# Kernel tuning notes

Measured on AMD Instinct MI355X. Metric: run time of the kernel, lower is better.

## Reference

```python
import jax, jax.numpy as jnp
import numpy as np

EPS = 1e-5

def _bn2d(x, g, b, m, v):
    s = (1, -1, 1, 1)
    return (x - m.reshape(s)) * (g.reshape(s) * jax.lax.rsqrt(v.reshape(s) + EPS)) + b.reshape(s)

def _bn1d(x, g, b, m, v):
    return (x - m) * (g * jax.lax.rsqrt(v + EPS)) + b

def _conv3x3(x, w, b):
    y = jax.lax.conv_general_dilated(x, w, (1, 1), ((1, 1), (1, 1)),
                                     dimension_numbers=('NCHW', 'OIHW', 'NCHW'))
    return y + b.reshape(1, -1, 1, 1)

def setup_inputs() -> dict:
    key = jax.random.key(0)
    ks = iter(jax.random.split(key, 64))
    B = 512
    d = {}
    d['anchor'] = jax.random.normal(next(ks), (B, 1, 16, 8), jnp.float32)
    d['positive'] = jax.random.normal(next(ks), (B, 1, 16, 8), jnp.float32)
    d['negative'] = jax.random.normal(next(ks), (B, 1, 16, 8), jnp.float32)

    def bn_params(c):
        g = jax.random.normal(next(ks), (c,), jnp.float32) * 0.1 + 1.0
        b = jax.random.normal(next(ks), (c,), jnp.float32) * 0.1
        m = jax.random.normal(next(ks), (c,), jnp.float32) * 0.1
        v = jax.random.uniform(next(ks), (c,), jnp.float32, 0.5, 1.5)
        return g, b, m, v

    d['bn0_g'], d['bn0_b'], d['bn0_m'], d['bn0_v'] = bn_params(1)
    d['conv1_w'] = jax.random.normal(next(ks), (64, 1, 3, 3), jnp.float32) * 0.1
    d['conv1_b'] = jax.random.normal(next(ks), (64,), jnp.float32) * 0.1
    d['bn1_g'], d['bn1_b'], d['bn1_m'], d['bn1_v'] = bn_params(64)
    d['conv2_w'] = jax.random.normal(next(ks), (64, 64, 3, 3), jnp.float32) * 0.04
    d['conv2_b'] = jax.random.normal(next(ks), (64,), jnp.float32) * 0.1
    d['bn2_g'], d['bn2_b'], d['bn2_m'], d['bn2_v'] = bn_params(64)
    # locally-connected: kernel_size=1 -> per-position unshared channel mix (o,c,h,w)
    d['lc1_w'] = jax.random.normal(next(ks), (64, 64, 16, 8), jnp.float32) * 0.125
    d['bn3_g'], d['bn3_b'], d['bn3_m'], d['bn3_v'] = bn_params(64)
    d['lc2_w'] = jax.random.normal(next(ks), (64, 64, 16, 8), jnp.float32) * 0.125
    d['bn4_g'], d['bn4_b'], d['bn4_m'], d['bn4_v'] = bn_params(64)
    d['fc1_w'] = jax.random.normal(next(ks), (512, 8192), jnp.float32) * 0.01
    d['fc1_b'] = jax.random.normal(next(ks), (512,), jnp.float32) * 0.1
    d['bnf1_g'], d['bnf1_b'], d['bnf1_m'], d['bnf1_v'] = bn_params(512)
    d['fc2_w'] = jax.random.normal(next(ks), (512, 512), jnp.float32) * 0.04
    d['fc2_b'] = jax.random.normal(next(ks), (512,), jnp.float32) * 0.1
    d['bnf2_g'], d['bnf2_b'], d['bnf2_m'], d['bnf2_v'] = bn_params(512)
    d['fc3_w'] = jax.random.normal(next(ks), (128, 512), jnp.float32) * 0.04
    d['fc3_b'] = jax.random.normal(next(ks), (128,), jnp.float32) * 0.1
    d['bnf3_g'], d['bnf3_b'], d['bnf3_m'], d['bnf3_v'] = bn_params(128)
    d['out_w'] = jax.random.normal(next(ks), (128, 128), jnp.float32) * 0.09
    d['out_b'] = jax.random.normal(next(ks), (128,), jnp.float32) * 0.1
    return d

def _embedding(x, p):
    x = _bn2d(x, p['bn0_g'], p['bn0_b'], p['bn0_m'], p['bn0_v'])
    x = _conv3x3(x, p['conv1_w'], p['conv1_b'])
    x = jax.nn.relu(_bn2d(x, p['bn1_g'], p['bn1_b'], p['bn1_m'], p['bn1_v']))
    x = _conv3x3(x, p['conv2_w'], p['conv2_b'])
    x = jax.nn.relu(_bn2d(x, p['bn2_g'], p['bn2_b'], p['bn2_m'], p['bn2_v']))
    # locally connected (kernel 1): per-position channel mix, no huge unfold intermediate
    x = jnp.einsum('bchw,ochw->bohw', x, p['lc1_w'])
    x = jax.nn.relu(_bn2d(x, p['bn3_g'], p['bn3_b'], p['bn3_m'], p['bn3_v']))
    x = jnp.einsum('bchw,ochw->bohw', x, p['lc2_w'])
    x = jax.nn.relu(_bn2d(x, p['bn4_g'], p['bn4_b'], p['bn4_m'], p['bn4_v']))
    # dropout is identity in eval mode
    x = x.reshape(x.shape[0], -1)  # (B, 8192)
    x = x @ p['fc1_w'].T + p['fc1_b']
    x = jax.nn.relu(_bn1d(x, p['bnf1_g'], p['bnf1_b'], p['bnf1_m'], p['bnf1_v']))
    x = x @ p['fc2_w'].T + p['fc2_b']
    x = jax.nn.relu(_bn1d(x, p['bnf2_g'], p['bnf2_b'], p['bnf2_m'], p['bnf2_v']))
    x = x @ p['fc3_w'].T + p['fc3_b']
    x = jax.nn.relu(_bn1d(x, p['bnf3_g'], p['bnf3_b'], p['bnf3_m'], p['bnf3_v']))
    return x @ p['out_w'].T + p['out_b']

def reference(anchor, positive, negative,
              bn0_g, bn0_b, bn0_m, bn0_v,
              conv1_w, conv1_b, bn1_g, bn1_b, bn1_m, bn1_v,
              conv2_w, conv2_b, bn2_g, bn2_b, bn2_m, bn2_v,
              lc1_w, bn3_g, bn3_b, bn3_m, bn3_v,
              lc2_w, bn4_g, bn4_b, bn4_m, bn4_v,
              fc1_w, fc1_b, bnf1_g, bnf1_b, bnf1_m, bnf1_v,
              fc2_w, fc2_b, bnf2_g, bnf2_b, bnf2_m, bnf2_v,
              fc3_w, fc3_b, bnf3_g, bnf3_b, bnf3_m, bnf3_v,
              out_w, out_b):
    p = dict(bn0_g=bn0_g, bn0_b=bn0_b, bn0_m=bn0_m, bn0_v=bn0_v,
             conv1_w=conv1_w, conv1_b=conv1_b, bn1_g=bn1_g, bn1_b=bn1_b, bn1_m=bn1_m, bn1_v=bn1_v,
             conv2_w=conv2_w, conv2_b=conv2_b, bn2_g=bn2_g, bn2_b=bn2_b, bn2_m=bn2_m, bn2_v=bn2_v,
             lc1_w=lc1_w, bn3_g=bn3_g, bn3_b=bn3_b, bn3_m=bn3_m, bn3_v=bn3_v,
             lc2_w=lc2_w, bn4_g=bn4_g, bn4_b=bn4_b, bn4_m=bn4_m, bn4_v=bn4_v,
             fc1_w=fc1_w, fc1_b=fc1_b, bnf1_g=bnf1_g, bnf1_b=bnf1_b, bnf1_m=bnf1_m, bnf1_v=bnf1_v,
             fc2_w=fc2_w, fc2_b=fc2_b, bnf2_g=bnf2_g, bnf2_b=bnf2_b, bnf2_m=bnf2_m, bnf2_v=bnf2_v,
             fc3_w=fc3_w, fc3_b=fc3_b, bnf3_g=bnf3_g, bnf3_b=bnf3_b, bnf3_m=bnf3_m, bnf3_v=bnf3_v,
             out_w=out_w, out_b=out_b)
    return (_embedding(anchor, p), _embedding(positive, p), _embedding(negative, p))
```

## Files before the change

### kernel.cpp

```cpp
#include <hip/hip_runtime.h>
#include <math.h>

#define EPS 1e-5f
#define FD 8192

typedef __attribute__((ext_vector_type(8))) __bf16 bf16x8;
typedef __attribute__((ext_vector_type(4))) float f32x4;

static __device__ __forceinline__ f32x4 mfma16(bf16x8 a, bf16x8 b, f32x4 c) {
    return __builtin_amdgcn_mfma_f32_16x16x32_bf16(a, b, c, 0, 0, 0);
}

__global__ __launch_bounds__(256) void k_prep_all(
    const float* __restrict__ w1, const float* __restrict__ w2,
    const float* __restrict__ lc1, const float* __restrict__ lc2,
    const float* __restrict__ fc1w, const float* __restrict__ fc2w,
    const float* __restrict__ fc3w, const float* __restrict__ outw,
    __bf16* __restrict__ w1frag, __bf16* __restrict__ w2frag,
    __bf16* __restrict__ lc1frag, __bf16* __restrict__ lc2frag,
    __bf16* __restrict__ fc1Wb, __bf16* __restrict__ wf23) {
    const int bb = blockIdx.x;
    const int t = threadIdx.x;
    __shared__ float wbuf[64][130];

    if (bb == 0) {
        const int lane = t & 63, w = t >> 6;
        const int q = lane >> 4, li = lane & 15;
        const int o = w * 16 + li;
        bf16x8 v;
#pragma unroll
        for (int j = 0; j < 8; ++j) {
            int k = q * 8 + j;
            v[j] = (k < 9) ? (__bf16)w1[o * 9 + k] : (__bf16)0.0f;
        }
        *(bf16x8*)(w1frag + t * 8) = v;
    } else if (bb < 19) {
        const int id = (bb - 1) * 256 + t;
        const int lane = id & 63;
        const int w = (id >> 6) & 3;
        const int chunk = (id >> 8) & 1;
        const int tap = id >> 9;
        const int q = lane >> 4, li = lane & 15;
        const int o = w * 16 + li;
        const int c0 = chunk * 32 + q * 8;
        bf16x8 v;
#pragma unroll
        for (int j = 0; j < 8; ++j)
            v[j] = (__bf16)w2[(o * 64 + c0 + j) * 9 + tap];
        *(bf16x8*)(w2frag + (size_t)id * 8) = v;
    } else if (bb < 147) {
        const int bx = bb - 19;
        const int layer = bx >> 6, o = bx & 63;
        const int wo = o >> 4, lo = o & 15;
        const float* src = (layer ? lc2 : lc1) + (size_t)o * 8192;
        __bf16* dst = layer ? lc2frag : lc1frag;
#pragma unroll
        for (int pass = 0; pass < 8; ++pass) {
            int i = pass * 1024 + t * 4;
            float4 v = *(const float4*)(src + i);
            int c = i >> 7, p = i & 127;
            wbuf[c][p + 0] = v.x; wbuf[c][p + 1] = v.y;
            wbuf[c][p + 2] = v.z; wbuf[c][p + 3] = v.w;
        }
        __syncthreads();
#pragma unroll
        for (int pass = 0; pass < 4; ++pass) {
            int slot = pass * 256 + t;
            int p = slot >> 3, chunk = (slot >> 2) & 1, q = slot & 3;
            bf16x8 v;
#pragma unroll
            for (int j = 0; j < 8; ++j)
                v[j] = (__bf16)wbuf[chunk * 32 + q * 8 + j][p];
            *(bf16x8*)(dst + ((size_t)((p * 2 + chunk) * 4 + wo) * 64 + q * 16 + lo) * 8) = v;
        }
    } else if (bb < 659) {
        const int n = bb - 147;
        const float* src = fc1w + (size_t)n * 8192;
        __bf16* dst = fc1Wb + (size_t)n * 8192;
#pragma unroll
        for (int pass = 0; pass < 8; ++pass) {
            int i = pass * 1024 + t * 4;
            float4 v = *(const float4*)(src + i);
            int c = i >> 7, p = i & 127;
            wbuf[c][p + 0] = v.x; wbuf[c][p + 1] = v.y;
            wbuf[c][p + 2] = v.z; wbuf[c][p + 3] = v.w;
        }
        __syncthreads();
#pragma unroll
        for (int pass = 0; pass < 16; ++pass) {
            int kA = (pass * 256 + t) * 2;
            int c = kA & 63, p = kA >> 6;
            __bf16 tmp[2];
            tmp[0] = (__bf16)wbuf[c][p];
            tmp[1] = (__bf16)wbuf[c + 1][p];
            *(unsigned int*)(dst + kA) = *(unsigned int*)tmp;
        }
    } else {
        int i = (bb - 659) * 256 + t;
        float v;
        if (i < 262144) v = fc2w[i];
        else if (i < 327680) v = fc3w[i - 262144];
        else v = outw[i - 327680];
        wf23[i] = (__bf16)v;
    }
}

__global__ __launch_bounds__(256) void k_conv_mfma(
    const float* __restrict__ inA, const float* __restrict__ inP, const float* __restrict__ inN,
    const float* __restrict__ bn0g, const float* __restrict__ bn0b,
    const float* __restrict__ bn0m, const float* __restrict__ bn0v,
    const __bf16* __restrict__ w1frag, const float* __restrict__ b1,
    const float* __restrict__ bn1g, const float* __restrict__ bn1b,
    const float* __restrict__ bn1m, const float* __restrict__ bn1v,
    const __bf16* __restrict__ w2frag, const float* __restrict__ b2,
    const float* __restrict__ bn2g, const float* __restrict__ bn2b,
    const float* __restrict__ bn2m, const float* __restrict__ bn2v,
    __bf16* __restrict__ act) {
    const int b = blockIdx.x, t = threadIdx.x;
    const int lane = t & 63, w = t >> 6;
    const int q = lane >> 4, li = lane & 15;
    const int n0 = w * 16;
    const float* src = (b < 512 ? inA : (b < 1024 ? inP : inN)) + (size_t)(b & 511) * 128;

    __shared__ __align__(16) float xpad[180];
    __shared__ __align__(16) __bf16 A1[128 * 40];
    __shared__ __align__(16) __bf16 Xp[18 * 12 * 72];
    __shared__ float s1[64], sh1[64], s2[64], sh2[64];

    bf16x8 w1f = *(const bf16x8*)(w1frag + (size_t)(w * 64 + lane) * 8);
    bf16x8 w2f[18];
#pragma unroll
    for (int tap = 0; tap < 9; ++tap)
#pragma unroll
        for (int ch = 0; ch < 2; ++ch)
            w2f[tap * 2 + ch] = *(const bf16x8*)(w2frag +
                ((size_t)((tap * 2 + ch) * 4 + w) * 64 + lane) * 8);

    {
        int* xz = (int*)Xp;
        for (int i = t; i < 7776; i += 256) xz[i] = 0;
        if (t < 180) xpad[t] = 0.f;
        if (t < 64) {
            float sa = bn1g[t] * rsqrtf(bn1v[t] + EPS);
            s1[t] = sa;
            sh1[t] = (b1[t] - bn1m[t]) * sa + bn1b[t];
            float sb = bn2g[t] * rsqrtf(bn2v[t] + EPS);
            s2[t] = sb;
            sh2[t] = (b2[t] - bn2m[t]) * sb + bn2b[t];
        }
    }
    __syncthreads();
    if (t < 128) {
        float s0 = bn0g[0] * rsqrtf(bn0v[0] + EPS);
        float v = (src[t] - bn0m[0]) * s0 + bn0b[0];
        xpad[((t >> 3) + 1) * 10 + (t & 7) + 1] = v;
    }
    __syncthreads();
    {
        int p = t >> 1, half = t & 1;
        int r = p >> 3, cl = p & 7;
        bf16x8 v0, v1;
#pragma unroll
        for (int jj = 0; jj < 8; ++jj) {
            int j = half * 16 + jj;
            v0[jj] = (j < 9) ? (__bf16)xpad[(r + j / 3) * 10 + cl + (j % 3)] : (__bf16)0.f;
            int j2 = half * 16 + 8 + jj;
            v1[jj] = (j2 < 9) ? (__bf16)xpad[(r + j2 / 3) * 10 + cl + (j2 % 3)] : (__bf16)0.f;
        }
        *(bf16x8*)&A1[p * 40 + half * 16] = v0;
        *(bf16x8*)&A1[p * 40 + half * 16 + 8] = v1;
    }
    __syncthreads();
    {
        const float sco = s1[n0 + li], sho = sh1[n0 + li];
        const int o = n0 + li;
#pragma unroll
        for (int m = 0; m < 8; ++m) {
            bf16x8 a = *(const bf16x8*)&A1[(m * 16 + li) * 40 + q * 8];
            f32x4 z = {0.f, 0.f, 0.f, 0.f};
            f32x4 d = mfma16(a, w1f, z);
#pragma unroll
            for (int r = 0; r < 4; ++r) {
                int p = m * 16 + q * 4 + r;
                float v = fmaxf(d[r] * sco + sho, 0.f);
                Xp[(((p >> 3) + 1) * 12 + (p & 7) + 1) * 72 + o] = (__bf16)v;
            }
        }
    }
    __syncthreads();
    f32x4 accA[4], accB[4];
#pragma unroll
    for (int i = 0; i < 4; ++i) {
        accA[i] = (f32x4){0.f, 0.f, 0.f, 0.f};
        accB[i] = (f32x4){0.f, 0.f, 0.f, 0.f};
    }
    {
        const int cl = li & 7;
#pragma unroll
        for (int mp = 0; mp < 4; ++mp) {
            const int r0 = mp * 4 + (li >> 3);
            const int base0 = (r0 * 12 + cl) * 72 + q * 8;
            const int base1 = base0 + 1728;
#pragma unroll
            for (int tap = 0; tap < 9; ++tap) {
                const int tofs = ((tap / 3) * 12 + (tap % 3)) * 72;
#pragma unroll
                for (int ch = 0; ch < 2; ++ch) {
                    bf16x8 a0 = *(const bf16x8*)&Xp[base0 + tofs + ch * 32];
                    bf16x8 a1 = *(const bf16x8*)&Xp[base1 + tofs + ch * 32];
                    accA[mp] = mfma16(a0, w2f[tap * 2 + ch], accA[mp]);
                    accB[mp] = mfma16(a1, w2f[tap * 2 + ch], accB[mp]);
                }
            }
        }
    }
    __syncthreads();
    {
        const float sco = s2[n0 + li], sho = sh2[n0 + li];
        const int o = n0 + li;
#pragma unroll
        for (int mp = 0; mp < 4; ++mp) {
#pragma unroll
            for (int r = 0; r < 4; ++r) {
                int p0 = mp * 32 + q * 4 + r;
                Xp[p0 * 72 + o] = (__bf16)fmaxf(accA[mp][r] * sco + sho, 0.f);
                Xp[(p0 + 16) * 72 + o] = (__bf16)fmaxf(accB[mp][r] * sco + sho, 0.f);
            }
        }
    }
    __syncthreads();
    {
        int p = t >> 1, half = t & 1;
        const __bf16* rp = Xp + p * 72 + half * 32;
        __bf16* ob = act + (size_t)b * FD + p * 64 + half * 32;
        bf16x8 v0 = *(const bf16x8*)rp;
        bf16x8 v1 = *(const bf16x8*)(rp + 8);
        bf16x8 v2 = *(const bf16x8*)(rp + 16);
        bf16x8 v3 = *(const bf16x8*)(rp + 24);
        *(bf16x8*)ob = v0;
        *(bf16x8*)(ob + 8) = v1;
        *(bf16x8*)(ob + 16) = v2;
        *(bf16x8*)(ob + 24) = v3;
    }
}

__global__ __launch_bounds__(256) void k_lc_mfma(
    const __bf16* __restrict__ lc1frag, const __bf16* __restrict__ lc2frag,
    const float* __restrict__ bn3g, const float* __restrict__ bn3b,
    const float* __restrict__ bn3m, const float* __restrict__ bn3v,
    const float* __restrict__ bn4g, const float* __restrict__ bn4b,
    const float* __restrict__ bn4m, const float* __restrict__ bn4v,
    __bf16* __restrict__ act) {
    const int p = blockIdx.x;
    const int b0 = blockIdx.y * 64;
    const int t = threadIdx.x;
    const int lane = t & 63, w = t >> 6;
    const int q = lane >> 4, li = lane & 15;
    const int n0 = w * 16;

    __shared__ __align__(16) __bf16 xs[64 * 72];
    __shared__ __align__(16) __bf16 ys[64 * 72];
    __shared__ float s3[64], sh3[64], s4[64], sh4[64];

    if (t < 64) {
        float sa = bn3g[t] * rsqrtf(bn3v[t] + EPS);
        s3[t] = sa; sh3[t] = bn3b[t] - bn3m[t] * sa;
        float sb = bn4g[t] * rsqrtf(bn4v[t] + EPS);
        s4[t] = sb; sh4[t] = bn4b[t] - bn4m[t] * sb;
    }
    {
        int s = t >> 2, cg = t & 3;
        const __bf16* rp = act + (size_t)(b0 + s) * FD + p * 64 + cg * 16;
        *(bf16x8*)&xs[s * 72 + cg * 16] = *(const bf16x8*)rp;
        *(bf16x8*)&xs[s * 72 + cg * 16 + 8] = *(const bf16x8*)(rp + 8);
    }
    bf16x8 w1a = *(const bf16x8*)(lc1frag + ((size_t)((p * 2 + 0) * 4 + w) * 64 + lane) * 8);
    bf16x8 w1b = *(const bf16x8*)(lc1frag + ((size_t)((p * 2 + 1) * 4 + w) * 64 + lane) * 8);
    bf16x8 w2a = *(const bf16x8*)(lc2frag + ((size_t)((p * 2 + 0) * 4 + w) * 64 + lane) * 8);
    bf16x8 w2b = *(const bf16x8*)(lc2frag + ((size_t)((p * 2 + 1) * 4 + w) * 64 + lane) * 8);
    __syncthreads();
    {
        const float sco = s3[n0 + li], sho = sh3[n0 + li];
#pragma unroll
        for (int m = 0; m < 4; ++m) {
            bf16x8 a0 = *(const bf16x8*)&xs[(m * 16 + li) * 72 + q * 8];
            bf16x8 a1 = *(const bf16x8*)&xs[(m * 16 + li) * 72 + 32 + q * 8];
            f32x4 acc = {0.f, 0.f, 0.f, 0.f};
            acc = mfma16(a0, w1a, acc);
            acc = mfma16(a1, w1b, acc);
#pragma unroll
            for (int r = 0; r < 4; ++r) {
                int bl = m * 16 + q * 4 + r;
                ys[bl * 72 + n0 + li] = (__bf16)fmaxf(acc[r] * sco + sho, 0.f);
            }
        }
    }
    __syncthreads();
    {
        const float sco = s4[n0 + li], sho = sh4[n0 + li];
#pragma unroll
        for (int m = 0; m < 4; ++m) {
            bf16x8 a0 = *(const bf16x8*)&ys[(m * 16 + li) * 72 + q * 8];
            bf16x8 a1 = *(const bf16x8*)&ys[(m * 16 + li) * 72 + 32 + q * 8];
            f32x4 acc = {0.f, 0.f, 0.f, 0.f};
            acc = mfma16(a0, w2a, acc);
            acc = mfma16(a1, w2b, acc);
#pragma unroll
            for (int r = 0; r < 4; ++r) {
                int bl = m * 16 + q * 4 + r;
                xs[bl * 72 + n0 + li] = (__bf16)fmaxf(acc[r] * sco + sho, 0.f);
            }
        }
    }
    __syncthreads();
    {
        int s = t >> 2, cg = t & 3;
        const __bf16* rp = xs + s * 72 + cg * 16;
        __bf16* ob = act + (size_t)(b0 + s) * FD + p * 64 + cg * 16;
        bf16x8 v0 = *(const bf16x8*)rp;
        bf16x8 v1 = *(const bf16x8*)(rp + 8);
        *(bf16x8*)ob = v0;
        *(bf16x8*)(ob + 8) = v1;
    }
}

__global__ __launch_bounds__(256) void k_fc1_mfma(
    const __bf16* __restrict__ A, const __bf16* __restrict__ Wb,
    float* __restrict__ part) {
    const int t = threadIdx.x;
    const int lane = t & 63, w = t >> 6;
    const int q = lane >> 4, li = lane & 15;
    const int m0 = blockIdx.x * 64, n0 = blockIdx.y * 128;
    const int k0 = blockIdx.z * 1024;
    const int wm = (w & 1) * 32, wn = (w >> 1) * 64;

    __shared__ __align__(16) __bf16 As[2][64 * 40];
    __shared__ __align__(16) __bf16 Bs[2][128 * 40];

    f32x4 acc[2][4];
#pragma unroll
    for (int i = 0; i < 2; ++i)
#pragma unroll
        for (int j = 0; j < 4; ++j) acc[i][j] = (f32x4){0.f, 0.f, 0.f, 0.f};

    const int rowA = (t & 127) >> 1, rowB = t >> 1, half = t & 1;
    const __bf16* Ag = A + (size_t)(m0 + rowA) * 8192 + k0 + half * 16;
    const __bf16* Bg = Wb + (size_t)(n0 + rowB) * 8192 + k0 + half * 16;

    bf16x8 pa0, pa1, pb0, pb1;
    pb0 = *(const bf16x8*)Bg;
    pb1 = *(const bf16x8*)(Bg + 8);
    if (t < 128) {
        pa0 = *(const bf16x8*)Ag;
        pa1 = *(const bf16x8*)(Ag + 8);
    }

    for (int step = 0; step < 32; ++step) {
        const int cur = step & 1;
        if (t < 128) {
            *(bf16x8*)&As[cur][rowA * 40 + half * 16] = pa0;
            *(bf16x8*)&As[cur][rowA * 40 + half * 16 + 8] = pa1;
        }
        *(bf16x8*)&Bs[cur][rowB * 40 + half * 16] = pb0;
        *(bf16x8*)&Bs[cur][rowB * 40 + half * 16 + 8] = pb1;
        __syncthreads();
        Ag += 32; Bg += 32;
        if (step < 31) {
            pb0 = *(const bf16x8*)Bg;
            pb1 = *(const bf16x8*)(Bg + 8);
            if (t < 128) {
                pa0 = *(const bf16x8*)Ag;
                pa1 = *(const bf16x8*)(Ag + 8);
            }
        }
        bf16x8 af[2], bfr[4];
#pragma unroll
        for (int i = 0; i < 2; ++i)
            af[i] = *(const bf16x8*)&As[cur][(wm + i * 16 + li) * 40 + q * 8];
#pragma unroll
        for (int j = 0; j < 4; ++j)
            bfr[j] = *(const bf16x8*)&Bs[cur][(wn + j * 16 + li) * 40 + q * 8];
#pragma unroll
        for (int i = 0; i < 2; ++i)
#pragma unroll
            for (int j = 0; j < 4; ++j)
                acc[i][j] = mfma16(af[i], bfr[j], acc[i][j]);
    }
    float* pp = part + (size_t)blockIdx.z * 786432;
#pragma unroll
    for (int i = 0; i < 2; ++i) {
#pragma unroll
        for (int r = 0; r < 4; ++r) {
            int m = m0 + wm + i * 16 + q * 4 + r;
#pragma unroll
            for (int j = 0; j < 4; ++j) {
                int n = n0 + wn + j * 16 + li;
                pp[(size_t)m * 512 + n] = acc[i][j][r];
            }
        }
    }
}

__global__ void k_fc1_reduce(const float* __restrict__ part, const float* __restrict__ bias,
                             const float* __restrict__ g, const float* __restrict__ bb,
                             const float* __restrict__ mm, const float* __restrict__ vv,
                             __bf16* __restrict__ out) {
    int gi = blockIdx.x * 256 + threadIdx.x;
    size_t off = (size_t)gi * 4;
    float4 s = make_float4(0.f, 0.f, 0.f, 0.f);
#pragma unroll
    for (int z = 0; z < 8; ++z) {
        float4 v = *(const float4*)(part + (size_t)z * 786432 + off);
        s.x += v.x; s.y += v.y; s.z += v.z; s.w += v.w;
    }
    int n = (gi & 127) * 4;
    float r[4] = {s.x, s.y, s.z, s.w};
    __bf16 o4[4];
#pragma unroll
    for (int j = 0; j < 4; ++j) {
        float sc = g[n + j] * rsqrtf(vv[n + j] + EPS);
        float x = (r[j] + bias[n + j] - mm[n + j]) * sc + bb[n + j];
        o4[j] = (__bf16)fmaxf(x, 0.f);
    }
    *(uint2*)(out + off) = *(uint2*)o4;
}

__global__ __launch_bounds__(256) void k_fc2_mfma(
    const __bf16* __restrict__ A, const __bf16* __restrict__ W,
    const float* __restrict__ bias,
    const float* __restrict__ bng, const float* __restrict__ bnb,
    const float* __restrict__ bnm, const float* __restrict__ bnv,
    __bf16* __restrict__ out) {
    const int t = threadIdx.x;
    const int lane = t & 63, w = t >> 6;
    const int q = lane >> 4, li = lane & 15;
    const int m0 = blockIdx.x * 64, n0 = blockIdx.y * 64;
    const int wm = (w & 1) * 32, wn = (w >> 1) * 32;
    const int K = 512, N = 512;

    __shared__ __align__(16) __bf16 As[2][64 * 40];
    __shared__ __align__(16) __bf16 Bs[2][64 * 40];

    f32x4 acc[2][2];
#pragma unroll
    for (int i = 0; i < 2; ++i)
#pragma unroll
        for (int j = 0; j < 2; ++j) acc[i][j] = (f32x4){0.f, 0.f, 0.f, 0.f};

    const int row = (t & 127) >> 1, half = t & 1;
    const __bf16* g = (t < 128 ? A + (size_t)(m0 + row) * K
                               : W + (size_t)(n0 + row) * K) + half * 16;
    const int ldo = row * 40 + half * 16;

    bf16x8 p0 = *(const bf16x8*)g;
    bf16x8 p1 = *(const bf16x8*)(g + 8);
    for (int s = 0; s < 16; ++s) {
        const int cur = s & 1;
        __bf16* ld = (t < 128 ? As[cur] : Bs[cur]) + ldo;
        *(bf16x8*)ld = p0;
        *(bf16x8*)(ld + 8) = p1;
        __syncthreads();
        g += 32;
        if (s < 15) {
            p0 = *(const bf16x8*)g;
            p1 = *(const bf16x8*)(g + 8);
        }
        bf16x8 af[2], bfr[2];
#pragma unroll
        for (int i = 0; i < 2; ++i)
            af[i] = *(const bf16x8*)&As[cur][(wm + i * 16 + li) * 40 + q * 8];
#pragma unroll
        for (int j = 0; j < 2; ++j)
            bfr[j] = *(const bf16x8*)&Bs[cur][(wn + j * 16 + li) * 40 + q * 8];
#pragma unroll
        for (int i = 0; i < 2; ++i)
#pragma unroll
            for (int j = 0; j < 2; ++j)
                acc[i][j] = mfma16(af[i], bfr[j], acc[i][j]);
    }
    float bi[2], sc[2], hh[2];
#pragma unroll
    for (int j = 0; j < 2; ++j) {
        int n = n0 + wn + j * 16 + li;
        bi[j] = bias[n];
        sc[j] = bng[n] * rsqrtf(bnv[n] + EPS);
        hh[j] = bnb[n] - bnm[n] * sc[j];
    }
#pragma unroll
    for (int i = 0; i < 2; ++i) {
#pragma unroll
        for (int r = 0; r < 4; ++r) {
            int m = m0 + wm + i * 16 + q * 4 + r;
#pragma unroll
            for (int j = 0; j < 2; ++j) {
                int n = n0 + wn + j * 16 + li;
                float x = (acc[i][j][r] + bi[j]) * sc[j] + hh[j];
                out[(size_t)m * N + n] = (__bf16)fmaxf(x, 0.f);
            }
        }
    }
}

__global__ __launch_bounds__(256) void k_fc3out(
    const __bf16* __restrict__ A, const __bf16* __restrict__ W3,
    const __bf16* __restrict__ Wo,
    const float* __restrict__ b3,
    const float* __restrict__ bng, const float* __restrict__ bnb,
    const float* __restrict__ bnm, const float* __restrict__ bnv,
    const float* __restrict__ bo, float* __restrict__ out) {
    const int t = threadIdx.x;
    const int lane = t & 63, w = t >> 6;
    const int q = lane >> 4, li = lane & 15;
    const int m0 = blockIdx.x * 32;
    const int wn = w * 32;

    __shared__ __align__(16) __bf16 As[2][32 * 40];
    __shared__ __align__(16) __bf16 Bs[2][128 * 40];
    __shared__ __align__(16) __bf16 ysb[32 * 136];

    const int rowA = (t & 63) >> 1, rowB = t >> 1, half = t & 1;
    const __bf16* Ag = A + (size_t)(m0 + rowA) * 512 + half * 16;
    const __bf16* Bg = W3 + (size_t)rowB * 512 + half * 16;

    f32x4 acc[2][2];
#pragma unroll
    for (int i = 0; i < 2; ++i)
#pragma unroll
        for (int j = 0; j < 2; ++j) acc[i][j] = (f32x4){0.f, 0.f, 0.f, 0.f};

    bf16x8 pa0, pa1, pb0, pb1;
    pb0 = *(const bf16x8*)Bg;
    pb1 = *(const bf16x8*)(Bg + 8);
    if (t < 64) {
        pa0 = *(const bf16x8*)Ag;
        pa1 = *(const bf16x8*)(Ag + 8);
    }
    for (int step = 0; step < 16; ++step) {
        const int cur = step & 1;
        if (t < 64) {
            *(bf16x8*)&As[cur][rowA * 40 + half * 16] = pa0;
            *(bf16x8*)&As[cur][rowA * 40 + half * 16 + 8] = pa1;
        }
        *(bf16x8*)&Bs[cur][rowB * 40 + half * 16] = pb0;
        *(bf16x8*)&Bs[cur][rowB * 40 + half * 16 + 8] = pb1;
        __syncthreads();
        Ag += 32; Bg += 32;
        if (step < 15) {
            pb0 = *(const bf16x8*)Bg;
            pb1 = *(const bf16x8*)(Bg + 8);
            if (t < 64) {
                pa0 = *(const bf16x8*)Ag;
                pa1 = *(const bf16x8*)(Ag + 8);
            }
        }
        bf16x8 af[2], bfr[2];
#pragma unroll
        for (int i = 0; i < 2; ++i)
            af[i] = *(const bf16x8*)&As[cur][(i * 16 + li) * 40 + q * 8];
#pragma unroll
        for (int j = 0; j < 2; ++j)
            bfr[j] = *(const bf16x8*)&Bs[cur][(wn + j * 16 + li) * 40 + q * 8];
#pragma unroll
        for (int i = 0; i < 2; ++i)
#pragma unroll
            for (int j = 0; j < 2; ++j)
                acc[i][j] = mfma16(af[i], bfr[j], acc[i][j]);
    }
    __syncthreads();
    {
#pragma unroll
        for (int j = 0; j < 2; ++j) {
            int n = wn + j * 16 + li;
            float sc = bng[n] * rsqrtf(bnv[n] + EPS);
            float hh = bnb[n] - bnm[n] * sc;
            float bi = b3[n];
#pragma unroll
            for (int i = 0; i < 2; ++i)
#pragma unroll
                for (int r = 0; r < 4; ++r) {
                    int ml = i * 16 + q * 4 + r;
                    float x = (acc[i][j][r] + bi) * sc + hh;
                    ysb[ml * 136 + n] = (__bf16)fmaxf(x, 0.f);
                }
        }
    }
    __syncthreads();
    f32x4 acc2[2][2];
#pragma unroll
    for (int i = 0; i < 2; ++i)
#pragma unroll
        for (int j = 0; j < 2; ++j) acc2[i][j] = (f32x4){0.f, 0.f, 0.f, 0.f};
    const __bf16* Bg2 = Wo + (size_t)rowB * 128 + half * 16;
#pragma unroll
    for (int s = 0; s < 4; ++s) {
        const int cur = s & 1;
        *(bf16x8*)&Bs[cur][rowB * 40 + half * 16] = *(const bf16x8*)(Bg2 + s * 32);
        *(bf16x8*)&Bs[cur][rowB * 40 + half * 16 + 8] = *(const bf16x8*)(Bg2 + s * 32 + 8);
        __syncthreads();
        bf16x8 af[2], bfr[2];
#pragma unroll
        for (int i = 0; i < 2; ++i)
            af[i] = *(const bf16x8*)&ysb[(i * 16 + li) * 136 + s * 32 + q * 8];
#pragma unroll
        for (int j = 0; j < 2; ++j)
            bfr[j] = *(const bf16x8*)&Bs[cur][(wn + j * 16 + li) * 40 + q * 8];
#pragma unroll
        for (int i = 0; i < 2; ++i)
#pragma unroll
            for (int j = 0; j < 2; ++j)
                acc2[i][j] = mfma16(af[i], bfr[j], acc2[i][j]);
    }
#pragma unroll
    for (int j = 0; j < 2; ++j) {
        int n = wn + j * 16 + li;
        float bi = bo[n];
#pragma unroll
        for (int i = 0; i < 2; ++i)
#pragma unroll
            for (int r = 0; r < 4; ++r) {
                int m = m0 + i * 16 + q * 4 + r;
                out[(size_t)m * 128 + n] = acc2[i][j][r] + bi;
            }
    }
}

extern "C" void kernel_launch(void* const* d_in, const int* in_sizes, int n_in,
                              void* d_out, int out_size, void* d_ws, size_t ws_size,
                              hipStream_t stream) {
    const float* inA    = (const float*)d_in[0];
    const float* inP    = (const float*)d_in[1];
    const float* inN    = (const float*)d_in[2];
    const float* bn0g   = (const float*)d_in[3];
    const float* bn0b   = (const float*)d_in[4];
    const float* bn0m   = (const float*)d_in[5];
    const float* bn0v   = (const float*)d_in[6];
    const float* conv1w = (const float*)d_in[7];
    const float* conv1b = (const float*)d_in[8];
    const float* bn1g   = (const float*)d_in[9];
    const float* bn1b   = (const float*)d_in[10];
    const float* bn1m   = (const float*)d_in[11];
    const float* bn1v   = (const float*)d_in[12];
    const float* conv2w = (const float*)d_in[13];
    const float* conv2b = (const float*)d_in[14];
    const float* bn2g   = (const float*)d_in[15];
    const float* bn2b   = (const float*)d_in[16];
    const float* bn2m   = (const float*)d_in[17];
    const float* bn2v   = (const float*)d_in[18];
    const float* lc1w   = (const float*)d_in[19];
    const float* bn3g   = (const float*)d_in[20];
    const float* bn3b   = (const float*)d_in[21];
    const float* bn3m   = (const float*)d_in[22];
    const float* bn3v   = (const float*)d_in[23];
    const float* lc2w   = (const float*)d_in[24];
    const float* bn4g   = (const float*)d_in[25];
    const float* bn4b   = (const float*)d_in[26];
    const float* bn4m   = (const float*)d_in[27];
    const float* bn4v   = (const float*)d_in[28];
    const float* fc1w   = (const float*)d_in[29];
    const float* fc1b   = (const float*)d_in[30];
    const float* bnf1g  = (const float*)d_in[31];
    const float* bnf1b  = (const float*)d_in[32];
    const float* bnf1m  = (const float*)d_in[33];
    const float* bnf1v  = (const float*)d_in[34];
    const float* fc2w   = (const float*)d_in[35];
    const float* fc2b   = (const float*)d_in[36];
    const float* bnf2g  = (const float*)d_in[37];
    const float* bnf2b  = (const float*)d_in[38];
    const float* bnf2m  = (const float*)d_in[39];
    const float* bnf2v  = (const float*)d_in[40];
    const float* fc3w   = (const float*)d_in[41];
    const float* fc3b   = (const float*)d_in[42];
    const float* bnf3g  = (const float*)d_in[43];
    const float* bnf3b  = (const float*)d_in[44];
    const float* bnf3m  = (const float*)d_in[45];
    const float* bnf3v  = (const float*)d_in[46];
    const float* outw   = (const float*)d_in[47];
    const float* outb   = (const float*)d_in[48];

    char* wsb = (char*)d_ws;
    __bf16* w1frag  = (__bf16*)wsb;
    __bf16* w2frag  = w1frag + 2048;
    __bf16* lc1frag = w2frag + 36864;
    __bf16* lc2frag = lc1frag + 524288;
    __bf16* fc1Wb   = lc2frag + 524288;
    __bf16* wf23    = fc1Wb + 4194304;
    __bf16* act     = wf23 + 344064;
    __bf16* act3    = act + 12582912;
    __bf16* act4    = act3 + 786432;
    float*  part    = (float*)(((uintptr_t)(act4 + 786432) + 15) & ~(uintptr_t)15);
    __bf16* wf2 = wf23;
    __bf16* wf3 = wf23 + 262144;
    __bf16* wfo = wf23 + 327680;

    k_prep_all<<<2003, 256, 0, stream>>>(conv1w, conv2w, lc1w, lc2w,
        fc1w, fc2w, fc3w, outw, w1frag, w2frag, lc1frag, lc2frag, fc1Wb, wf23);

    k_conv_mfma<<<1536, 256, 0, stream>>>(inA, inP, inN,
        bn0g, bn0b, bn0m, bn0v, w1frag, conv1b, bn1g, bn1b, bn1m, bn1v,
        w2frag, conv2b, bn2g, bn2b, bn2m, bn2v, act);

    k_lc_mfma<<<dim3(128, 24), 256, 0, stream>>>(lc1frag, lc2frag,
        bn3g, bn3b, bn3m, bn3v, bn4g, bn4b, bn4m, bn4v, act);

    k_fc1_mfma<<<dim3(24, 4, 8), 256, 0, stream>>>(act, fc1Wb, part);
    k_fc1_reduce<<<768, 256, 0, stream>>>(part, fc1b, bnf1g, bnf1b, bnf1m, bnf1v, act3);

    k_fc2_mfma<<<dim3(24, 8), 256, 0, stream>>>(act3, wf2, fc2b,
        bnf2g, bnf2b, bnf2m, bnf2v, act4);

    k_fc3out<<<48, 256, 0, stream>>>(act4, wf3, wfo, fc3b,
        bnf3g, bnf3b, bnf3m, bnf3v, outb, (float*)d_out);
}
```

Baseline: 248.9 us.

## Fuse weight prep into conv kernel, enlarge LC batch tile, halve fc1 split-K

Result: slower. 268.6 us (+7.9%).

```diff
diff --git a/kernel.cpp b/kernel.cpp
--- a/kernel.cpp
+++ b/kernel.cpp
@@ -11,18 +11,11 @@
     return __builtin_amdgcn_mfma_f32_16x16x32_bf16(a, b, c, 0, 0, 0);
 }
 
-__global__ __launch_bounds__(256) void k_prep_all(
+__global__ __launch_bounds__(256) void k_prep_conv(
     const float* __restrict__ w1, const float* __restrict__ w2,
-    const float* __restrict__ lc1, const float* __restrict__ lc2,
-    const float* __restrict__ fc1w, const float* __restrict__ fc2w,
-    const float* __restrict__ fc3w, const float* __restrict__ outw,
-    __bf16* __restrict__ w1frag, __bf16* __restrict__ w2frag,
-    __bf16* __restrict__ lc1frag, __bf16* __restrict__ lc2frag,
-    __bf16* __restrict__ fc1Wb, __bf16* __restrict__ wf23) {
+    __bf16* __restrict__ w1frag, __bf16* __restrict__ w2frag) {
     const int bb = blockIdx.x;
     const int t = threadIdx.x;
-    __shared__ float wbuf[64][130];
-
     if (bb == 0) {
         const int lane = t & 63, w = t >> 6;
         const int q = lane >> 4, li = lane & 15;
@@ -34,7 +27,7 @@
             v[j] = (k < 9) ? (__bf16)w1[o * 9 + k] : (__bf16)0.0f;
         }
         *(bf16x8*)(w1frag + t * 8) = v;
-    } else if (bb < 19) {
+    } else {
         const int id = (bb - 1) * 256 + t;
         const int lane = id & 63;
         const int w = (id >> 6) & 3;
@@ -48,64 +41,10 @@
         for (int j = 0; j < 8; ++j)
             v[j] = (__bf16)w2[(o * 64 + c0 + j) * 9 + tap];
         *(bf16x8*)(w2frag + (size_t)id * 8) = v;
-    } else if (bb < 147) {
-        const int bx = bb - 19;
-        const int layer = bx >> 6, o = bx & 63;
-        const int wo = o >> 4, lo = o & 15;
-        const float* src = (layer ? lc2 : lc1) + (size_t)o * 8192;
-        __bf16* dst = layer ? lc2frag : lc1frag;
-#pragma unroll
-        for (int pass = 0; pass < 8; ++pass) {
-            int i = pass * 1024 + t * 4;
-            float4 v = *(const float4*)(src + i);
-            int c = i >> 7, p = i & 127;
-            wbuf[c][p + 0] = v.x; wbuf[c][p + 1] = v.y;
-            wbuf[c][p + 2] = v.z; wbuf[c][p + 3] = v.w;
-        }
-        __syncthreads();
-#pragma unroll
-        for (int pass = 0; pass < 4; ++pass) {
-            int slot = pass * 256 + t;
-            int p = slot >> 3, chunk = (slot >> 2) & 1, q = slot & 3;
-            bf16x8 v;
-#pragma unroll
-            for (int j = 0; j < 8; ++j)
-                v[j] = (__bf16)wbuf[chunk * 32 + q * 8 + j][p];
-            *(bf16x8*)(dst + ((size_t)((p * 2 + chunk) * 4 + wo) * 64 + q * 16 + lo) * 8) = v;
-        }
-    } else if (bb < 659) {
-        const int n = bb - 147;
-        const float* src = fc1w + (size_t)n * 8192;
-        __bf16* dst = fc1Wb + (size_t)n * 8192;
-#pragma unroll
-        for (int pass = 0; pass < 8; ++pass) {
-            int i = pass * 1024 + t * 4;
-            float4 v = *(const float4*)(src + i);
-            int c = i >> 7, p = i & 127;
-            wbuf[c][p + 0] = v.x; wbuf[c][p + 1] = v.y;
-            wbuf[c][p + 2] = v.z; wbuf[c][p + 3] = v.w;
-        }
-        __syncthreads();
-#pragma unroll
-        for (int pass = 0; pass < 16; ++pass) {
-            int kA = (pass * 256 + t) * 2;
-            int c = kA & 63, p = kA >> 6;
-            __bf16 tmp[2];
-            tmp[0] = (__bf16)wbuf[c][p];
-            tmp[1] = (__bf16)wbuf[c + 1][p];
-            *(unsigned int*)(dst + kA) = *(unsigned int*)tmp;
-        }
-    } else {
-        int i = (bb - 659) * 256 + t;
-        float v;
-        if (i < 262144) v = fc2w[i];
-        else if (i < 327680) v = fc3w[i - 262144];
-        else v = outw[i - 327680];
-        wf23[i] = (__bf16)v;
-    }
-}
-
-__global__ __launch_bounds__(256) void k_conv_mfma(
+    }
+}
+
+__global__ __launch_bounds__(256) void k_conv_prep(
     const float* __restrict__ inA, const float* __restrict__ inP, const float* __restrict__ inN,
     const float* __restrict__ bn0g, const float* __restrict__ bn0b,
     const float* __restrict__ bn0m, const float* __restrict__ bn0v,
@@ -115,17 +54,97 @@
     const __bf16* __restrict__ w2frag, const float* __restrict__ b2,
     const float* __restrict__ bn2g, const float* __restrict__ bn2b,
     const float* __restrict__ bn2m, const float* __restrict__ bn2v,
-    __bf16* __restrict__ act) {
-    const int b = blockIdx.x, t = threadIdx.x;
+    __bf16* __restrict__ act,
+    const float* __restrict__ lc1, const float* __restrict__ lc2,
+    const float* __restrict__ fc1w, const float* __restrict__ fc2w,
+    const float* __restrict__ fc3w, const float* __restrict__ outw,
+    __bf16* __restrict__ lc1frag, __bf16* __restrict__ lc2frag,
+    __bf16* __restrict__ fc1Wb, __bf16* __restrict__ wf23) {
+    const int bb = blockIdx.x;
+    const int t = threadIdx.x;
+    __shared__ __align__(16) char smem[43136];
+
+    if (bb >= 1536) {
+        const int bx2 = bb - 1536;
+        if (bx2 < 128) {
+            float (*wbuf)[68] = (float(*)[68])smem;
+            const int layer = bx2 >> 6, o = bx2 & 63;
+            const int wo = o >> 4, lo = o & 15;
+            const float* src = (layer ? lc2 : lc1) + (size_t)o * 8192;
+            __bf16* dst = layer ? lc2frag : lc1frag;
+            for (int P = 0; P < 2; ++P) {
+                if (P) __syncthreads();
+#pragma unroll
+                for (int it = 0; it < 4; ++it) {
+                    int idx = it * 1024 + t * 4;
+                    int c = idx >> 6, pp = idx & 63;
+                    float4 v = *(const float4*)(src + c * 128 + P * 64 + pp);
+                    wbuf[c][pp + 0] = v.x; wbuf[c][pp + 1] = v.y;
+                    wbuf[c][pp + 2] = v.z; wbuf[c][pp + 3] = v.w;
+                }
+                __syncthreads();
+#pragma unroll
+                for (int it = 0; it < 2; ++it) {
+                    int slot = it * 256 + t;
+                    int pp = slot >> 3, chunk = (slot >> 2) & 1, q = slot & 3;
+                    int p = P * 64 + pp;
+                    bf16x8 v;
+#pragma unroll
+                    for (int j = 0; j < 8; ++j)
+                        v[j] = (__bf16)wbuf[chunk * 32 + q * 8 + j][pp];
+                    *(bf16x8*)(dst + ((size_t)((p * 2 + chunk) * 4 + wo) * 64 + q * 16 + lo) * 8) = v;
+                }
+            }
+        } else if (bx2 < 640) {
+            float (*wbuf)[68] = (float(*)[68])smem;
+            const int n = bx2 - 128;
+            const float* src = fc1w + (size_t)n * 8192;
+            __bf16* dst = fc1Wb + (size_t)n * 8192;
+            for (int P = 0; P < 2; ++P) {
+                if (P) __syncthreads();
+#pragma unroll
+                for (int it = 0; it < 4; ++it) {
+                    int idx = it * 1024 + t * 4;
+                    int c = idx >> 6, pp = idx & 63;
+                    float4 v = *(const float4*)(src + c * 128 + P * 64 + pp);
+                    wbuf[c][pp + 0] = v.x; wbuf[c][pp + 1] = v.y;
+                    wbuf[c][pp + 2] = v.z; wbuf[c][pp + 3] = v.w;
+                }
+                __syncthreads();
+#pragma unroll
+                for (int it = 0; it < 8; ++it) {
+                    int kA = P * 4096 + (it * 256 + t) * 2;
+                    int c = kA & 63, pp = (kA >> 6) & 63;
+                    __bf16 tmp[2];
+                    tmp[0] = (__bf16)wbuf[c][pp];
+                    tmp[1] = (__bf16)wbuf[c + 1][pp];
+                    *(unsigned int*)(dst + kA) = *(unsigned int*)tmp;
+                }
+            }
+        } else {
+            int i = (bx2 - 640) * 256 + t;
+            float v;
+            if (i < 262144) v = fc2w[i];
+            else if (i < 327680) v = fc3w[i - 262144];
+            else v = outw[i - 327680];
+            wf23[i] = (__bf16)v;
+        }
+        return;
+    }
+
+    float* xpad = (float*)smem;
+    __bf16* A1  = (__bf16*)(smem + 768);
+    __bf16* Xp  = (__bf16*)(smem + 11008);
+    float* s1   = (float*)(smem + 42112);
+    float* sh1  = (float*)(smem + 42368);
+    float* s2   = (float*)(smem + 42624);
+    float* sh2  = (float*)(smem + 42880);
+
+    const int b = bb;
     const int lane = t & 63, w = t >> 6;
     const int q = lane >> 4, li = lane & 15;
     const int n0 = w * 16;
     const float* src = (b < 512 ? inA : (b < 1024 ? inP : inN)) + (size_t)(b & 511) * 128;
-
-    __shared__ __align__(16) float xpad[180];
-    __shared__ __align__(16) __bf16 A1[128 * 40];
-    __shared__ __align__(16) __bf16 Xp[18 * 12 * 72];
-    __shared__ float s1[64], sh1[64], s2[64], sh2[64];
 
     bf16x8 w1f = *(const bf16x8*)(w1frag + (size_t)(w * 64 + lane) * 8);
     bf16x8 w2f[18];
@@ -252,14 +271,14 @@
     const float* __restrict__ bn4m, const float* __restrict__ bn4v,
     __bf16* __restrict__ act) {
     const int p = blockIdx.x;
-    const int b0 = blockIdx.y * 64;
+    const int b0 = blockIdx.y * 128;
     const int t = threadIdx.x;
     const int lane = t & 63, w = t >> 6;
     const int q = lane >> 4, li = lane & 15;
     const int n0 = w * 16;
 
-    __shared__ __align__(16) __bf16 xs[64 * 72];
-    __shared__ __align__(16) __bf16 ys[64 * 72];
+    __shared__ __align__(16) __bf16 xs[128 * 72];
+    __shared__ __align__(16) __bf16 ys[128 * 72];
     __shared__ float s3[64], sh3[64], s4[64], sh4[64];
 
     if (t < 64) {
@@ -269,10 +288,12 @@
         s4[t] = sb; sh4[t] = bn4b[t] - bn4m[t] * sb;
     }
     {
-        int s = t >> 2, cg = t & 3;
-        const __bf16* rp = act + (size_t)(b0 + s) * FD + p * 64 + cg * 16;
-        *(bf16x8*)&xs[s * 72 + cg * 16] = *(const bf16x8*)rp;
-        *(bf16x8*)&xs[s * 72 + cg * 16 + 8] = *(const bf16x8*)(rp + 8);
+        int s = t >> 1, cg = t & 1;
+        const __bf16* rp = act + (size_t)(b0 + s) * FD + p * 64 + cg * 32;
+        *(bf16x8*)&xs[s * 72 + cg * 32] = *(const bf16x8*)rp;
+        *(bf16x8*)&xs[s * 72 + cg * 32 + 8] = *(const bf16x8*)(rp + 8);
+        *(bf16x8*)&xs[s * 72 + cg * 32 + 16] = *(const bf16x8*)(rp + 16);
+        *(bf16x8*)&xs[s * 72 + cg * 32 + 24] = *(const bf16x8*)(rp + 24);
     }
     bf16x8 w1a = *(const bf16x8*)(lc1frag + ((size_t)((p * 2 + 0) * 4 + w) * 64 + lane) * 8);
     bf16x8 w1b = *(const bf16x8*)(lc1frag + ((size_t)((p * 2 + 1) * 4 + w) * 64 + lane) * 8);
@@ -282,7 +303,7 @@
     {
         const float sco = s3[n0 + li], sho = sh3[n0 + li];
 #pragma unroll
-        for (int m = 0; m < 4; ++m) {
+        for (int m = 0; m < 8; ++m) {
             bf16x8 a0 = *(const bf16x8*)&xs[(m * 16 + li) * 72 + q * 8];
             bf16x8 a1 = *(const bf16x8*)&xs[(m * 16 + li) * 72 + 32 + q * 8];
             f32x4 acc = {0.f, 0.f, 0.f, 0.f};
@@ -299,7 +320,7 @@
     {
         const float sco = s4[n0 + li], sho = sh4[n0 + li];
 #pragma unroll
-        for (int m = 0; m < 4; ++m) {
+        for (int m = 0; m < 8; ++m) {
             bf16x8 a0 = *(const bf16x8*)&ys[(m * 16 + li) * 72 + q * 8];
             bf16x8 a1 = *(const bf16x8*)&ys[(m * 16 + li) * 72 + 32 + q * 8];
             f32x4 acc = {0.f, 0.f, 0.f, 0.f};
@@ -314,13 +335,17 @@
     }
     __syncthreads();
     {
-        int s = t >> 2, cg = t & 3;
-        const __bf16* rp = xs + s * 72 + cg * 16;
-        __bf16* ob = act + (size_t)(b0 + s) * FD + p * 64 + cg * 16;
+        int s = t >> 1, cg = t & 1;
+        const __bf16* rp = xs + s * 72 + cg * 32;
+        __bf16* ob = act + (size_t)(b0 + s) * FD + p * 64 + cg * 32;
         bf16x8 v0 = *(const bf16x8*)rp;
         bf16x8 v1 = *(const bf16x8*)(rp + 8);
+        bf16x8 v2 = *(const bf16x8*)(rp + 16);
+        bf16x8 v3 = *(const bf16x8*)(rp + 24);
         *(bf16x8*)ob = v0;
         *(bf16x8*)(ob + 8) = v1;
+        *(bf16x8*)(ob + 16) = v2;
+        *(bf16x8*)(ob + 24) = v3;
     }
 }
 
@@ -331,7 +356,7 @@
     const int lane = t & 63, w = t >> 6;
     const int q = lane >> 4, li = lane & 15;
     const int m0 = blockIdx.x * 64, n0 = blockIdx.y * 128;
-    const int k0 = blockIdx.z * 1024;
+    const int k0 = blockIdx.z * 2048;
     const int wm = (w & 1) * 32, wn = (w >> 1) * 64;
 
     __shared__ __align__(16) __bf16 As[2][64 * 40];
@@ -355,7 +380,7 @@
         pa1 = *(const bf16x8*)(Ag + 8);
     }
 
-    for (int step = 0; step < 32; ++step) {
+    for (int step = 0; step < 64; ++step) {
         const int cur = step & 1;
         if (t < 128) {
             *(bf16x8*)&As[cur][rowA * 40 + half * 16] = pa0;
@@ -365,7 +390,7 @@
         *(bf16x8*)&Bs[cur][rowB * 40 + half * 16 + 8] = pb1;
         __syncthreads();
         Ag += 32; Bg += 32;
-        if (step < 31) {
+        if (step < 63) {
             pb0 = *(const bf16x8*)Bg;
             pb1 = *(const bf16x8*)(Bg + 8);
             if (t < 128) {
@@ -409,7 +434,7 @@
     size_t off = (size_t)gi * 4;
     float4 s = make_float4(0.f, 0.f, 0.f, 0.f);
 #pragma unroll
-    for (int z = 0; z < 8; ++z) {
+    for (int z = 0; z < 4; ++z) {
         float4 v = *(const float4*)(part + (size_t)z * 786432 + off);
         s.x += v.x; s.y += v.y; s.z += v.z; s.w += v.w;
     }
@@ -692,17 +717,18 @@
     __bf16* wf3 = wf23 + 262144;
     __bf16* wfo = wf23 + 327680;
 
-    k_prep_all<<<2003, 256, 0, stream>>>(conv1w, conv2w, lc1w, lc2w,
-        fc1w, fc2w, fc3w, outw, w1frag, w2frag, lc1frag, lc2frag, fc1Wb, wf23);
-
-    k_conv_mfma<<<1536, 256, 0, stream>>>(inA, inP, inN,
+    k_prep_conv<<<19, 256, 0, stream>>>(conv1w, conv2w, w1frag, w2frag);
+
+    k_conv_prep<<<3520, 256, 0, stream>>>(inA, inP, inN,
         bn0g, bn0b, bn0m, bn0v, w1frag, conv1b, bn1g, bn1b, bn1m, bn1v,
-        w2frag, conv2b, bn2g, bn2b, bn2m, bn2v, act);
-
-    k_lc_mfma<<<dim3(128, 24), 256, 0, stream>>>(lc1frag, lc2frag,
+        w2frag, conv2b, bn2g, bn2b, bn2m, bn2v, act,
+        lc1w, lc2w, fc1w, fc2w, fc3w, outw,
+        lc1frag, lc2frag, fc1Wb, wf23);
+
+    k_lc_mfma<<<dim3(128, 12), 256, 0, stream>>>(lc1frag, lc2frag,
         bn3g, bn3b, bn3m, bn3v, bn4g, bn4b, bn4m, bn4v, act);
 
-    k_fc1_mfma<<<dim3(24, 4, 8), 256, 0, stream>>>(act, fc1Wb, part);
+    k_fc1_mfma<<<dim3(24, 4, 4), 256, 0, stream>>>(act, fc1Wb, part);
     k_fc1_reduce<<<768, 256, 0, stream>>>(part, fc1b, bnf1g, bnf1b, bnf1m, bnf1v, act3);
 
     k_fc2_mfma<<<dim3(24, 8), 256, 0, stream>>>(act3, wf2, fc2b,
```
